# Kernel tuning notes

Measured on AMD Instinct MI355X. Metric: run time of the kernel, lower is better.

The kernel has to match this reference:

```python
import jax, jax.numpy as jnp
import numpy as np

N0, N1, N2 = 400000, 40000, 4000   # source nodes, layer-1 targets, layer-2 targets
E1, E2 = 640000, 64000             # sampled edges per bipartite block (avg deg 16)
IN, HID, OUT = 128, 256, 64


def setup_inputs() -> dict:
    key = jax.random.key(0)
    ks = jax.random.split(key, 11)
    x = jax.random.normal(ks[0], (N0, IN), jnp.float32)
    src1 = jax.random.randint(ks[1], (E1,), 0, N0)
    dst1 = jax.random.randint(ks[2], (E1,), 0, N1)
    src2 = jax.random.randint(ks[3], (E2,), 0, N1)
    dst2 = jax.random.randint(ks[4], (E2,), 0, N2)
    # SAGEConv params (PyG default: mean aggr, lin_l on aggregated msgs w/ bias, lin_r on root)
    s_in, s_hid = 1.0 / np.sqrt(IN), 1.0 / np.sqrt(HID)
    w_l1 = jax.random.uniform(ks[5], (IN, HID), jnp.float32, -s_in, s_in)
    b_l1 = jnp.zeros((HID,), jnp.float32)
    w_r1 = jax.random.uniform(ks[6], (IN, HID), jnp.float32, -s_in, s_in)
    w_l2 = jax.random.uniform(ks[7], (HID, OUT), jnp.float32, -s_hid, s_hid)
    b_l2 = jnp.zeros((OUT,), jnp.float32)
    w_r2 = jax.random.uniform(ks[8], (HID, OUT), jnp.float32, -s_hid, s_hid)
    return dict(x=x, src1=src1, dst1=dst1, src2=src2, dst2=dst2,
                w_l1=w_l1, b_l1=b_l1, w_r1=w_r1,
                w_l2=w_l2, b_l2=b_l2, w_r2=w_r2,
                n1=N1, n2=N2)


def _sage_conv(x_src, x_tgt, src, dst, w_l, b_l, w_r, n_tgt):
    # mean aggregation of neighbor features onto targets
    msg = x_src[src]                                             # [E, F] gather
    agg = jax.ops.segment_sum(msg, dst, num_segments=n_tgt)      # [n_tgt, F] scatter-add
    deg = jax.ops.segment_sum(jnp.ones_like(dst, x_src.dtype), dst, num_segments=n_tgt)
    agg = agg / jnp.maximum(deg, 1.0)[:, None]
    return agg @ w_l + b_l + x_tgt @ w_r


def reference(x, src1, dst1, src2, dst2, w_l1, b_l1, w_r1, w_l2, b_l2, w_r2, n1, n2):
    # layer 1: bipartite block (N0 sources -> n1 targets), targets are prefix of sources
    h = _sage_conv(x, x[:n1], src1, dst1, w_l1, b_l1, w_r1, n1)
    h = jax.nn.relu(h)  # eval mode: dropout is identity
    # layer 2: (n1 sources -> n2 targets)
    out = _sage_conv(h, h[:n2], src2, dst2, w_l2, b_l2, w_r2, n2)
    return jax.nn.log_softmax(out, axis=-1)
```

## Files before the change

kernel.cpp:

```cpp
#include <hip/hip_runtime.h>
#include <math.h>

#define IN   128
#define HID  256
#define OUT  64
#define N0   400000
#define N1T  40000
#define N2T  4000
#define E1   640000
#define E2   64000

__global__ __launch_bounds__(256) void hist_kernel(
    const int* __restrict__ dst1, const int* __restrict__ dst2,
    int* __restrict__ cnt1, int* __restrict__ cnt2)
{
    int e = blockIdx.x * 256 + threadIdx.x;
    if (e < E1) {
        atomicAdd(&cnt1[dst1[e]], 1);
    } else if (e < E1 + E2) {
        atomicAdd(&cnt2[dst2[e - E1]], 1);
    }
}

__global__ __launch_bounds__(1024) void scan2_kernel(
    const int* __restrict__ cnt1, int* __restrict__ off1, int* __restrict__ cur1,
    const int* __restrict__ cnt2, int* __restrict__ off2, int* __restrict__ cur2)
{
    const int* cnt; int* off; int* cur; int n;
    if (blockIdx.x == 0) { cnt = cnt1; off = off1; cur = cur1; n = N1T; }
    else                 { cnt = cnt2; off = off2; cur = cur2; n = N2T; }

    __shared__ int sums[1024];
    const int t = threadIdx.x;
    const int chunk = (n + 1023) >> 10;
    const int begin = min(t * chunk, n);
    const int end = min(begin + chunk, n);

    int s = 0;
    for (int i = begin; i < end; ++i) s += cnt[i];
    sums[t] = s;
    __syncthreads();

    for (int d = 1; d < 1024; d <<= 1) {
        int tmp = (t >= d) ? sums[t - d] : 0;
        __syncthreads();
        sums[t] += tmp;
        __syncthreads();
    }

    int run = sums[t] - s;
    for (int i = begin; i < end; ++i) {
        off[i] = run;
        cur[i] = run;
        run += cnt[i];
    }
    if (end == n && begin < end) off[n] = run;
}

__global__ __launch_bounds__(256) void scatter_idx_kernel(
    const int* __restrict__ src1, const int* __restrict__ dst1,
    const int* __restrict__ src2, const int* __restrict__ dst2,
    int* __restrict__ cur1, int* __restrict__ cur2,
    int* __restrict__ ss1, int* __restrict__ ss2)
{
    int e = blockIdx.x * 256 + threadIdx.x;
    if (e < E1) {
        int pos = atomicAdd(&cur1[dst1[e]], 1);
        ss1[pos] = src1[e];
    } else if (e < E1 + E2) {
        int ee = e - E1;
        int pos = atomicAdd(&cur2[dst2[ee]], 1);
        ss2[pos] = src2[ee];
    }
}

__global__ __launch_bounds__(256) void gather1_kernel(
    const float* __restrict__ x,
    const int* __restrict__ off, const int* __restrict__ ss,
    float* __restrict__ agg)
{
    int row = blockIdx.x * 4 + (threadIdx.x >> 6);
    if (row >= N1T) return;
    int lane = threadIdx.x & 63;
    int b = off[row], en = off[row + 1];

    float2 acc = make_float2(0.0f, 0.0f);
    for (int base = b; base < en; base += 64) {
        int cnt = min(64, en - base);
        int myidx = (lane < cnt) ? ss[base + lane] : 0;
        int e = 0;
        for (; e + 4 <= cnt; e += 4) {
            int s0 = __shfl(myidx, e);
            int s1 = __shfl(myidx, e + 1);
            int s2 = __shfl(myidx, e + 2);
            int s3 = __shfl(myidx, e + 3);
            float2 v0 = reinterpret_cast<const float2*>(x + (size_t)s0 * IN)[lane];
            float2 v1 = reinterpret_cast<const float2*>(x + (size_t)s1 * IN)[lane];
            float2 v2 = reinterpret_cast<const float2*>(x + (size_t)s2 * IN)[lane];
            float2 v3 = reinterpret_cast<const float2*>(x + (size_t)s3 * IN)[lane];
            acc.x += v0.x + v1.x + v2.x + v3.x;
            acc.y += v0.y + v1.y + v2.y + v3.y;
        }
        for (; e < cnt; ++e) {
            int s = __shfl(myidx, e);
            float2 v = reinterpret_cast<const float2*>(x + (size_t)s * IN)[lane];
            acc.x += v.x;
            acc.y += v.y;
        }
    }
    float inv = 1.0f / fmaxf((float)(en - b), 1.0f);
    acc.x *= inv;
    acc.y *= inv;
    reinterpret_cast<float2*>(agg + (size_t)row * IN)[lane] = acc;
}

__global__ __launch_bounds__(256) void gather2_kernel(
    const float* __restrict__ h,
    const int* __restrict__ off, const int* __restrict__ ss,
    float* __restrict__ agg)
{
    int row = blockIdx.x * 4 + (threadIdx.x >> 6);
    if (row >= N2T) return;
    int lane = threadIdx.x & 63;
    int b = off[row], en = off[row + 1];

    float4 acc = make_float4(0.0f, 0.0f, 0.0f, 0.0f);
    for (int base = b; base < en; base += 64) {
        int cnt = min(64, en - base);
        int myidx = (lane < cnt) ? ss[base + lane] : 0;
        int e = 0;
        for (; e + 2 <= cnt; e += 2) {
            int s0 = __shfl(myidx, e);
            int s1 = __shfl(myidx, e + 1);
            float4 v0 = reinterpret_cast<const float4*>(h + (size_t)s0 * HID)[lane];
            float4 v1 = reinterpret_cast<const float4*>(h + (size_t)s1 * HID)[lane];
            acc.x += v0.x + v1.x; acc.y += v0.y + v1.y;
            acc.z += v0.z + v1.z; acc.w += v0.w + v1.w;
        }
        for (; e < cnt; ++e) {
            int s = __shfl(myidx, e);
            float4 v = reinterpret_cast<const float4*>(h + (size_t)s * HID)[lane];
            acc.x += v.x; acc.y += v.y; acc.z += v.z; acc.w += v.w;
        }
    }
    float inv = 1.0f / fmaxf((float)(en - b), 1.0f);
    acc.x *= inv; acc.y *= inv; acc.z *= inv; acc.w *= inv;
    reinterpret_cast<float4*>(agg + (size_t)row * HID)[lane] = acc;
}

__global__ __launch_bounds__(256) void layer1_kernel(
    const float* __restrict__ x,
    const float* __restrict__ agg,
    const float* __restrict__ w_l, const float* __restrict__ b_l,
    const float* __restrict__ w_r, float* __restrict__ h)
{
    __shared__ float A_s[256][64];
    const int r0 = blockIdx.x * 64;
    const int tid = threadIdx.x;

    for (int i = tid; i < 64 * 32; i += 256) {
        int r = i >> 5;
        int c4 = i & 31;
        float4 va = reinterpret_cast<const float4*>(agg + (size_t)(r0 + r) * IN)[c4];
        float4 vx = reinterpret_cast<const float4*>(x + (size_t)(r0 + r) * IN)[c4];
        int k = c4 * 4;
        A_s[k + 0][r] = va.x; A_s[k + 1][r] = va.y;
        A_s[k + 2][r] = va.z; A_s[k + 3][r] = va.w;
        A_s[128 + k + 0][r] = vx.x; A_s[128 + k + 1][r] = vx.y;
        A_s[128 + k + 2][r] = vx.z; A_s[128 + k + 3][r] = vx.w;
    }
    __syncthreads();

    const int ngrp = tid & 63;
    const int mgrp = tid >> 6;

    float acc[16][4];
#pragma unroll
    for (int m = 0; m < 16; ++m)
#pragma unroll
        for (int j = 0; j < 4; ++j) acc[m][j] = 0.0f;

    const float4* wl4 = reinterpret_cast<const float4*>(w_l);
    const float4* wr4 = reinterpret_cast<const float4*>(w_r);

#pragma unroll 4
    for (int k = 0; k < 128; ++k) {
        float4 w = wl4[k * 64 + ngrp];
        const float4* ap = reinterpret_cast<const float4*>(&A_s[k][mgrp * 16]);
        float4 a0 = ap[0], a1 = ap[1], a2 = ap[2], a3 = ap[3];
        float am[16] = {a0.x, a0.y, a0.z, a0.w, a1.x, a1.y, a1.z, a1.w,
                        a2.x, a2.y, a2.z, a2.w, a3.x, a3.y, a3.z, a3.w};
#pragma unroll
        for (int m = 0; m < 16; ++m) {
            acc[m][0] += am[m] * w.x;
            acc[m][1] += am[m] * w.y;
            acc[m][2] += am[m] * w.z;
            acc[m][3] += am[m] * w.w;
        }
    }
#pragma unroll 4
    for (int k = 0; k < 128; ++k) {
        float4 w = wr4[k * 64 + ngrp];
        const float4* ap = reinterpret_cast<const float4*>(&A_s[128 + k][mgrp * 16]);
        float4 a0 = ap[0], a1 = ap[1], a2 = ap[2], a3 = ap[3];
        float am[16] = {a0.x, a0.y, a0.z, a0.w, a1.x, a1.y, a1.z, a1.w,
                        a2.x, a2.y, a2.z, a2.w, a3.x, a3.y, a3.z, a3.w};
#pragma unroll
        for (int m = 0; m < 16; ++m) {
            acc[m][0] += am[m] * w.x;
            acc[m][1] += am[m] * w.y;
            acc[m][2] += am[m] * w.z;
            acc[m][3] += am[m] * w.w;
        }
    }

    float4 b = reinterpret_cast<const float4*>(b_l)[ngrp];
#pragma unroll
    for (int m = 0; m < 16; ++m) {
        float4 o;
        o.x = fmaxf(acc[m][0] + b.x, 0.0f);
        o.y = fmaxf(acc[m][1] + b.y, 0.0f);
        o.z = fmaxf(acc[m][2] + b.z, 0.0f);
        o.w = fmaxf(acc[m][3] + b.w, 0.0f);
        reinterpret_cast<float4*>(h + (size_t)(r0 + mgrp * 16 + m) * HID)[ngrp] = o;
    }
}

__global__ __launch_bounds__(64) void layer2_kernel(
    const float* __restrict__ h,
    const float* __restrict__ agg,
    const float* __restrict__ w_l, const float* __restrict__ b_l,
    const float* __restrict__ w_r, float* __restrict__ out)
{
    __shared__ float a_s[HID];
    __shared__ float h_s[HID];
    const int i = blockIdx.x;
    const int j = threadIdx.x;

    const float4* ar = reinterpret_cast<const float4*>(agg + (size_t)i * HID);
    const float4* hr = reinterpret_cast<const float4*>(h + (size_t)i * HID);
    reinterpret_cast<float4*>(a_s)[j] = ar[j];
    reinterpret_cast<float4*>(h_s)[j] = hr[j];
    __syncthreads();

    float acc = b_l[j];
    for (int k = 0; k < HID; ++k) {
        acc += a_s[k] * w_l[k * OUT + j] + h_s[k] * w_r[k * OUT + j];
    }

    float m = acc;
#pragma unroll
    for (int off = 32; off; off >>= 1) m = fmaxf(m, __shfl_xor(m, off));
    float ex = expf(acc - m);
#pragma unroll
    for (int off = 32; off; off >>= 1) ex += __shfl_xor(ex, off);
    out[(size_t)i * OUT + j] = acc - m - logf(ex);
}

extern "C" void kernel_launch(void* const* d_in, const int* in_sizes, int n_in,
                              void* d_out, int out_size, void* d_ws, size_t ws_size,
                              hipStream_t stream)
{
    const float* x    = (const float*)d_in[0];
    const int*   src1 = (const int*)  d_in[1];
    const int*   dst1 = (const int*)  d_in[2];
    const int*   src2 = (const int*)  d_in[3];
    const int*   dst2 = (const int*)  d_in[4];
    const float* w_l1 = (const float*)d_in[5];
    const float* b_l1 = (const float*)d_in[6];
    const float* w_r1 = (const float*)d_in[7];
    const float* w_l2 = (const float*)d_in[8];
    const float* b_l2 = (const float*)d_in[9];
    const float* w_r2 = (const float*)d_in[10];
    float* out = (float*)d_out;

    int* ws_i = (int*)d_ws;
    int* cnt1 = ws_i;
    int* cnt2 = cnt1 + N1T;
    int* off1 = cnt2 + N2T;
    int* off2 = off1 + N1T + 1;
    int* cur1 = off2 + N2T + 1;
    int* cur2 = cur1 + N1T;
    int* ss1  = cur2 + N2T;
    int* ss2  = ss1 + E1;
    float* agg1 = (float*)(ss2 + E2);
    float* agg2 = agg1 + (size_t)N1T * IN;
    float* h    = agg2 + (size_t)N2T * HID;

    hipMemsetAsync(cnt1, 0, (N1T + N2T) * sizeof(int), stream);

    const int ET = E1 + E2;
    hist_kernel<<<(ET + 255) / 256, 256, 0, stream>>>(dst1, dst2, cnt1, cnt2);
    scan2_kernel<<<2, 1024, 0, stream>>>(cnt1, off1, cur1, cnt2, off2, cur2);
    scatter_idx_kernel<<<(ET + 255) / 256, 256, 0, stream>>>(src1, dst1, src2, dst2,
                                                             cur1, cur2, ss1, ss2);
    gather1_kernel<<<(N1T + 3) / 4, 256, 0, stream>>>(x, off1, ss1, agg1);
    layer1_kernel<<<N1T / 64, 256, 0, stream>>>(x, agg1, w_l1, b_l1, w_r1, h);
    gather2_kernel<<<(N2T + 3) / 4, 256, 0, stream>>>(h, off2, ss2, agg2);
    layer2_kernel<<<N2T, 64, 0, stream>>>(h, agg2, w_l2, b_l2, w_r2, out);
}
```

Before: 604.8 us.

## Fuse neighbor mean-aggregation into layer GEMM kernels, dropping agg buffers

Folds the gather/mean-aggregation into the layer-1 GEMM kernel, writing averaged rows straight into shared memory, and into the layer-2 per-row kernel. This removes the agg1/agg2 global round trips and two launches. It also pads the shared tile to 68 columns. The cost is that layer 1 now has only 625 blocks, each doing 64 rows of serialized gathers, so the gather stage gets much less parallelism and latency hiding than the previous 10000-block gather kernel.

```diff
diff --git a/kernel.cpp b/kernel.cpp
--- a/kernel.cpp
+++ b/kernel.cpp
@@ -74,100 +74,59 @@
     }
 }
 
-__global__ __launch_bounds__(256) void gather1_kernel(
+__global__ __launch_bounds__(256) void layer1_fused_kernel(
     const float* __restrict__ x,
     const int* __restrict__ off, const int* __restrict__ ss,
-    float* __restrict__ agg)
-{
-    int row = blockIdx.x * 4 + (threadIdx.x >> 6);
-    if (row >= N1T) return;
-    int lane = threadIdx.x & 63;
-    int b = off[row], en = off[row + 1];
-
-    float2 acc = make_float2(0.0f, 0.0f);
-    for (int base = b; base < en; base += 64) {
-        int cnt = min(64, en - base);
-        int myidx = (lane < cnt) ? ss[base + lane] : 0;
-        int e = 0;
-        for (; e + 4 <= cnt; e += 4) {
-            int s0 = __shfl(myidx, e);
-            int s1 = __shfl(myidx, e + 1);
-            int s2 = __shfl(myidx, e + 2);
-            int s3 = __shfl(myidx, e + 3);
-            float2 v0 = reinterpret_cast<const float2*>(x + (size_t)s0 * IN)[lane];
-            float2 v1 = reinterpret_cast<const float2*>(x + (size_t)s1 * IN)[lane];
-            float2 v2 = reinterpret_cast<const float2*>(x + (size_t)s2 * IN)[lane];
-            float2 v3 = reinterpret_cast<const float2*>(x + (size_t)s3 * IN)[lane];
-            acc.x += v0.x + v1.x + v2.x + v3.x;
-            acc.y += v0.y + v1.y + v2.y + v3.y;
-        }
-        for (; e < cnt; ++e) {
-            int s = __shfl(myidx, e);
-            float2 v = reinterpret_cast<const float2*>(x + (size_t)s * IN)[lane];
-            acc.x += v.x;
-            acc.y += v.y;
-        }
-    }
-    float inv = 1.0f / fmaxf((float)(en - b), 1.0f);
-    acc.x *= inv;
-    acc.y *= inv;
-    reinterpret_cast<float2*>(agg + (size_t)row * IN)[lane] = acc;
-}
-
-__global__ __launch_bounds__(256) void gather2_kernel(
-    const float* __restrict__ h,
-    const int* __restrict__ off, const int* __restrict__ ss,
-    float* __restrict__ agg)
-{
-    int row = blockIdx.x * 4 + (threadIdx.x >> 6);
-    if (row >= N2T) return;
-    int lane = threadIdx.x & 63;
-    int b = off[row], en = off[row + 1];
-
-    float4 acc = make_float4(0.0f, 0.0f, 0.0f, 0.0f);
-    for (int base = b; base < en; base += 64) {
-        int cnt = min(64, en - base);
-        int myidx = (lane < cnt) ? ss[base + lane] : 0;
-        int e = 0;
-        for (; e + 2 <= cnt; e += 2) {
-            int s0 = __shfl(myidx, e);
-            int s1 = __shfl(myidx, e + 1);
-            float4 v0 = reinterpret_cast<const float4*>(h + (size_t)s0 * HID)[lane];
-            float4 v1 = reinterpret_cast<const float4*>(h + (size_t)s1 * HID)[lane];
-            acc.x += v0.x + v1.x; acc.y += v0.y + v1.y;
-            acc.z += v0.z + v1.z; acc.w += v0.w + v1.w;
-        }
-        for (; e < cnt; ++e) {
-            int s = __shfl(myidx, e);
-            float4 v = reinterpret_cast<const float4*>(h + (size_t)s * HID)[lane];
-            acc.x += v.x; acc.y += v.y; acc.z += v.z; acc.w += v.w;
-        }
-    }
-    float inv = 1.0f / fmaxf((float)(en - b), 1.0f);
-    acc.x *= inv; acc.y *= inv; acc.z *= inv; acc.w *= inv;
-    reinterpret_cast<float4*>(agg + (size_t)row * HID)[lane] = acc;
-}
-
-__global__ __launch_bounds__(256) void layer1_kernel(
-    const float* __restrict__ x,
-    const float* __restrict__ agg,
     const float* __restrict__ w_l, const float* __restrict__ b_l,
     const float* __restrict__ w_r, float* __restrict__ h)
 {
-    __shared__ float A_s[256][64];
+    __shared__ __align__(16) float A_s[256][68];
     const int r0 = blockIdx.x * 64;
     const int tid = threadIdx.x;
+    const int lane = tid & 63;
+    const int wv = tid >> 6;
 
     for (int i = tid; i < 64 * 32; i += 256) {
         int r = i >> 5;
         int c4 = i & 31;
-        float4 va = reinterpret_cast<const float4*>(agg + (size_t)(r0 + r) * IN)[c4];
         float4 vx = reinterpret_cast<const float4*>(x + (size_t)(r0 + r) * IN)[c4];
-        int k = c4 * 4;
-        A_s[k + 0][r] = va.x; A_s[k + 1][r] = va.y;
-        A_s[k + 2][r] = va.z; A_s[k + 3][r] = va.w;
-        A_s[128 + k + 0][r] = vx.x; A_s[128 + k + 1][r] = vx.y;
-        A_s[128 + k + 2][r] = vx.z; A_s[128 + k + 3][r] = vx.w;
+        int k = 128 + c4 * 4;
+        A_s[k + 0][r] = vx.x; A_s[k + 1][r] = vx.y;
+        A_s[k + 2][r] = vx.z; A_s[k + 3][r] = vx.w;
+    }
+
+    for (int i = 0; i < 16; ++i) {
+        int r = wv * 16 + i;
+        int row = r0 + r;
+        int b = off[row], en = off[row + 1];
+
+        float2 acc = make_float2(0.0f, 0.0f);
+        for (int base = b; base < en; base += 64) {
+            int cnt = min(64, en - base);
+            int myidx = (lane < cnt) ? ss[base + lane] : 0;
+            int e = 0;
+            for (; e + 4 <= cnt; e += 4) {
+                int s0 = __shfl(myidx, e);
+                int s1 = __shfl(myidx, e + 1);
+                int s2 = __shfl(myidx, e + 2);
+                int s3 = __shfl(myidx, e + 3);
+                float2 v0 = reinterpret_cast<const float2*>(x + (size_t)s0 * IN)[lane];
+                float2 v1 = reinterpret_cast<const float2*>(x + (size_t)s1 * IN)[lane];
+                float2 v2 = reinterpret_cast<const float2*>(x + (size_t)s2 * IN)[lane];
+                float2 v3 = reinterpret_cast<const float2*>(x + (size_t)s3 * IN)[lane];
+                acc.x += v0.x + v1.x + v2.x + v3.x;
+                acc.y += v0.y + v1.y + v2.y + v3.y;
+            }
+            for (; e < cnt; ++e) {
+                int s = __shfl(myidx, e);
+                float2 v = reinterpret_cast<const float2*>(x + (size_t)s * IN)[lane];
+                acc.x += v.x;
+                acc.y += v.y;
+            }
+        }
+        float inv = 1.0f / fmaxf((float)(en - b), 1.0f);
+        A_s[2 * lane][r]     = acc.x * inv;
+        A_s[2 * lane + 1][r] = acc.y * inv;
     }
     __syncthreads();
 
@@ -226,21 +185,43 @@
     }
 }
 
-__global__ __launch_bounds__(64) void layer2_kernel(
-    const float* __restrict__ h,
-    const float* __restrict__ agg,
+__global__ __launch_bounds__(64) void layer2_fused_kernel(
+    const float* __restrict__ hsrc,
+    const int* __restrict__ off, const int* __restrict__ ss,
     const float* __restrict__ w_l, const float* __restrict__ b_l,
     const float* __restrict__ w_r, float* __restrict__ out)
 {
-    __shared__ float a_s[HID];
-    __shared__ float h_s[HID];
+    __shared__ __align__(16) float a_s[HID];
+    __shared__ __align__(16) float h_s[HID];
     const int i = blockIdx.x;
     const int j = threadIdx.x;
 
-    const float4* ar = reinterpret_cast<const float4*>(agg + (size_t)i * HID);
-    const float4* hr = reinterpret_cast<const float4*>(h + (size_t)i * HID);
-    reinterpret_cast<float4*>(a_s)[j] = ar[j];
-    reinterpret_cast<float4*>(h_s)[j] = hr[j];
+    reinterpret_cast<float4*>(h_s)[j] =
+        reinterpret_cast<const float4*>(hsrc + (size_t)i * HID)[j];
+
+    int b = off[i], en = off[i + 1];
+    float4 acc4 = make_float4(0.0f, 0.0f, 0.0f, 0.0f);
+    for (int base = b; base < en; base += 64) {
+        int cnt = min(64, en - base);
+        int myidx = (j < cnt) ? ss[base + j] : 0;
+        int e = 0;
+        for (; e + 2 <= cnt; e += 2) {
+            int s0 = __shfl(myidx, e);
+            int s1 = __shfl(myidx, e + 1);
+            float4 v0 = reinterpret_cast<const float4*>(hsrc + (size_t)s0 * HID)[j];
+            float4 v1 = reinterpret_cast<const float4*>(hsrc + (size_t)s1 * HID)[j];
+            acc4.x += v0.x + v1.x; acc4.y += v0.y + v1.y;
+            acc4.z += v0.z + v1.z; acc4.w += v0.w + v1.w;
+        }
+        for (; e < cnt; ++e) {
+            int s = __shfl(myidx, e);
+            float4 v = reinterpret_cast<const float4*>(hsrc + (size_t)s * HID)[j];
+            acc4.x += v.x; acc4.y += v.y; acc4.z += v.z; acc4.w += v.w;
+        }
+    }
+    float inv = 1.0f / fmaxf((float)(en - b), 1.0f);
+    acc4.x *= inv; acc4.y *= inv; acc4.z *= inv; acc4.w *= inv;
+    reinterpret_cast<float4*>(a_s)[j] = acc4;
     __syncthreads();
 
     float acc = b_l[j];
@@ -250,10 +231,10 @@
 
     float m = acc;
 #pragma unroll
-    for (int off = 32; off; off >>= 1) m = fmaxf(m, __shfl_xor(m, off));
+    for (int off2 = 32; off2; off2 >>= 1) m = fmaxf(m, __shfl_xor(m, off2));
     float ex = expf(acc - m);
 #pragma unroll
-    for (int off = 32; off; off >>= 1) ex += __shfl_xor(ex, off);
+    for (int off2 = 32; off2; off2 >>= 1) ex += __shfl_xor(ex, off2);
     out[(size_t)i * OUT + j] = acc - m - logf(ex);
 }
 
@@ -283,9 +264,7 @@
     int* cur2 = cur1 + N1T;
     int* ss1  = cur2 + N2T;
     int* ss2  = ss1 + E1;
-    float* agg1 = (float*)(ss2 + E2);
-    float* agg2 = agg1 + (size_t)N1T * IN;
-    float* h    = agg2 + (size_t)N2T * HID;
+    float* h  = (float*)(ss2 + E2);
 
     hipMemsetAsync(cnt1, 0, (N1T + N2T) * sizeof(int), stream);
 
@@ -294,8 +273,6 @@
     scan2_kernel<<<2, 1024, 0, stream>>>(cnt1, off1, cur1, cnt2, off2, cur2);
     scatter_idx_kernel<<<(ET + 255) / 256, 256, 0, stream>>>(src1, dst1, src2, dst2,
                                                              cur1, cur2, ss1, ss2);
-    gather1_kernel<<<(N1T + 3) / 4, 256, 0, stream>>>(x, off1, ss1, agg1);
-    layer1_kernel<<<N1T / 64, 256, 0, stream>>>(x, agg1, w_l1, b_l1, w_r1, h);
-    gather2_kernel<<<(N2T + 3) / 4, 256, 0, stream>>>(h, off2, ss2, agg2);
-    layer2_kernel<<<N2T, 64, 0, stream>>>(h, agg2, w_l2, b_l2, w_r2, out);
-}
+    layer1_fused_kernel<<<N1T / 64, 256, 0, stream>>>(x, off1, ss1, w_l1, b_l1, w_r1, h);
+    layer2_fused_kernel<<<N2T, 64, 0, stream>>>(h, off2, ss2, w_l2, b_l2, w_r2, out);
+}
```

Result: slower. 649.5 us (+7.4%).
